# Kernel optimization log

Hardware: AMD Instinct MI355X
Metric: run time of the kernel (lower is better)

The kernel has to match this reference:

```python
import jax, jax.numpy as jnp
import numpy as np

HEADS = 12
DIM_HEAD = 64
WINDOW = 16
SHIFT = 1  # fixed stand-in for random.randint(0, window-1)
SCALE = DIM_HEAD ** -0.5


def window_cls_mask(n, window, shift):
    # Shifted block-diagonal mask over the n-1 non-CLS tokens, CLS attends/attended everywhere.
    size = n - 1
    idx = jnp.arange(size)
    cur = (idx - shift) % window
    left = jnp.clip(idx - cur, 0, size)
    right = jnp.clip(idx + (window - cur), 0, size)
    i = idx[:, None]  # query position
    wmask = (i >= left[None, :]) & (i < right[None, :])  # [size, size]
    full = jnp.ones((n, n), dtype=bool)
    full = full.at[1:, 1:].set(wmask)
    return full  # [n, n] bool


def setup_inputs() -> dict:
    key = jax.random.key(0)
    k1, k2, k3 = jax.random.split(key, 3)
    b, n, dim = 2, 2049, 768
    inner = HEADS * DIM_HEAD
    return {
        "x": jax.random.normal(k1, (b, n, dim), dtype=jnp.float32),
        "w_qkv": jax.random.normal(k2, (dim, 3 * inner), dtype=jnp.float32) * 0.02,
        "w_out": jax.random.normal(k3, (inner, dim), dtype=jnp.float32) * 0.02,
        "b_out": jnp.zeros((dim,), dtype=jnp.float32),
    }


def reference(x, w_qkv, w_out, b_out):
    b, n, dim = x.shape
    h, d = HEADS, DIM_HEAD
    qkv = x @ w_qkv  # [b, n, 3*h*d]
    q, k, v = jnp.split(qkv, 3, axis=-1)
    # b n (h d) -> b h n d
    reshape = lambda t: t.reshape(b, n, h, d).transpose(0, 2, 1, 3)
    q, k, v = reshape(q), reshape(k), reshape(v)
    dots = jnp.einsum('bhid,bhjd->bhij', q, k) * SCALE  # [b, h, n, n]
    mask = window_cls_mask(n, WINDOW, SHIFT)  # [n, n]
    neg = -jnp.finfo(dots.dtype).max
    dots = jnp.where(mask[None, None], dots, neg)
    attn = jax.nn.softmax(dots, axis=-1)
    out = jnp.einsum('bhij,bhjd->bhid', attn, v)  # [b, h, n, d]
    out = out.transpose(0, 2, 1, 3).reshape(b, n, h * d)
    return out @ w_out + b_out
```

## Files before the change

### kernel.cpp

```cpp
#include <hip/hip_runtime.h>
#include <hip/hip_bf16.h>
#include <math.h>

typedef __attribute__((ext_vector_type(8))) __bf16 bf16x8;
typedef __attribute__((ext_vector_type(4))) float f32x4;

#define HEADS 12
#define DHEAD 64
#define NTOK 2049
#define BATCH 2
#define DIM 768
#define QKV3 2304
#define MROWS 4098
#define MP 4224
#define ATT_SCALE 0.125f
#define BKS 64
#define NSPLIT 33
#define PSTRIDE 68

#define CVT_BLOCKS 1584
#define TQKV_BX 72
#define TQKV_BLOCKS (72 * 24)
#define TOUT_BX 24
#define TOUT_BLOCKS (24 * 24)
#define PREP_BLOCKS (CVT_BLOCKS + TQKV_BLOCKS + TOUT_BLOCKS)
#define WIN_BLOCKS (BATCH * 129 * 3)

__device__ __forceinline__ int xcd_swz(int o, int nwg) {
  const int q = nwg >> 3, r = nwg & 7;
  const int xcd = o & 7, i = o >> 3;
  return (xcd < r ? xcd * (q + 1) : r * (q + 1) + (xcd - r) * q) + i;
}

__global__ __launch_bounds__(256) void prep_kernel(const float* __restrict__ x,
                                                   const float* __restrict__ w_qkv,
                                                   const float* __restrict__ w_out,
                                                   __bf16* __restrict__ xb,
                                                   __bf16* __restrict__ wqkvT,
                                                   __bf16* __restrict__ woutT) {
  __shared__ float tile[32][33];
  const int b = blockIdx.x, tid = threadIdx.x;
  if (b < CVT_BLOCKS) {
    long e = ((long)b * 256 + tid) * 8;
    int row = (int)(e / DIM);
    bf16x8 v;
    if (row < MROWS) {
      const float4 a = *(const float4*)(x + e);
      const float4 c = *(const float4*)(x + e + 4);
      v[0] = (__bf16)a.x; v[1] = (__bf16)a.y; v[2] = (__bf16)a.z; v[3] = (__bf16)a.w;
      v[4] = (__bf16)c.x; v[5] = (__bf16)c.y; v[6] = (__bf16)c.z; v[7] = (__bf16)c.w;
    } else {
#pragma unroll
      for (int j = 0; j < 8; ++j) v[j] = (__bf16)0.f;
    }
    *(bf16x8*)(xb + e) = v;
    return;
  }
  const float* in;
  __bf16* outp;
  int C, bx, by;
  if (b < CVT_BLOCKS + TQKV_BLOCKS) {
    int idx = b - CVT_BLOCKS;
    bx = idx % TQKV_BX; by = idx / TQKV_BX;
    in = w_qkv; outp = wqkvT; C = QKV3;
  } else {
    int idx = b - CVT_BLOCKS - TQKV_BLOCKS;
    bx = idx % TOUT_BX; by = idx / TOUT_BX;
    in = w_out; outp = woutT; C = DIM;
  }
  const int R = DIM;
  const int c0 = bx * 32, r0 = by * 32;
  const int tx = tid & 31, ty = tid >> 5;
#pragma unroll
  for (int i = 0; i < 4; ++i) {
    int r = ty + i * 8;
    tile[r][tx] = in[(size_t)(r0 + r) * C + c0 + tx];
  }
  __syncthreads();
#pragma unroll
  for (int i = 0; i < 4; ++i) {
    int r = ty + i * 8;
    outp[(size_t)(c0 + r) * R + r0 + tx] = (__bf16)tile[tx][r];
  }
}

__global__ __launch_bounds__(256) void gemm_qkv_kernel(const __bf16* __restrict__ A,
                                                       const __bf16* __restrict__ Bt,
                                                       __bf16* __restrict__ C) {
  __shared__ __bf16 sA[2][64 * BKS];
  __shared__ __bf16 sB[2][128 * BKS];
  const int wg = xcd_swz(blockIdx.x, (MP / 64) * (QKV3 / 128));
  const int by = wg / (QKV3 / 128), bx = wg % (QKV3 / 128);
  const int tid = threadIdx.x;
  const int w = tid >> 6, lane = tid & 63;
  const int m0 = by * 64, n0 = bx * 128;
  const int wr = w >> 1, wc = w & 1;
  const int K = DIM;
  f32x4 acc[2][4] = {};

  const int srow = (w << 3) + (lane >> 3);
  const int scolE = ((lane & 7) ^ (lane >> 3)) << 3;
  const __bf16* gA = A + (size_t)(m0 + srow) * K + scolE;
  const __bf16* gB = Bt + (size_t)(n0 + srow) * K + scolE;
  const int nk = K / BKS;

#define STAGE_Q(buf, kt)                                                                 \
  do {                                                                                   \
    _Pragma("unroll")                                                                    \
    for (int it = 0; it < 2; ++it) {                                                     \
      __builtin_amdgcn_global_load_lds(                                                  \
          (const __attribute__((address_space(1))) void*)(gA + (size_t)(it * 32) * K + (kt)), \
          (__attribute__((address_space(3))) void*)(&sA[buf][(it << 11) + (w << 9)]), 16, 0, 0); \
    }                                                                                    \
    _Pragma("unroll")                                                                    \
    for (int it = 0; it < 4; ++it) {                                                     \
      __builtin_amdgcn_global_load_lds(                                                  \
          (const __attribute__((address_space(1))) void*)(gB + (size_t)(it * 32) * K + (kt)), \
          (__attribute__((address_space(3))) void*)(&sB[buf][(it << 11) + (w << 9)]), 16, 0, 0); \
    }                                                                                    \
  } while (0)

  STAGE_Q(0, 0);
  __syncthreads();

  const int sw0 = ((lane >> 4) ^ (lane & 7)) << 3;
  const int sw1 = sw0 ^ 32;
  const int rofA = (wr * 32 + (lane & 15)) * BKS;
  const int rofB = (wc * 64 + (lane & 15)) * BKS;

  for (int t = 0; t < nk; ++t) {
    const int cur = t & 1;
    if (t + 1 < nk) STAGE_Q(cur ^ 1, (t + 1) * BKS);
    const __bf16* bufA = sA[cur];
    const __bf16* bufB = sB[cur];
#pragma unroll
    for (int kk = 0; kk < BKS; kk += 32) {
      const int so = (kk == 0) ? sw0 : sw1;
      bf16x8 af[2], bfr[4];
#pragma unroll
      for (int m = 0; m < 2; ++m)
        af[m] = *(const bf16x8*)&bufA[rofA + m * 16 * BKS + so];
#pragma unroll
      for (int n = 0; n < 4; ++n)
        bfr[n] = *(const bf16x8*)&bufB[rofB + n * 16 * BKS + so];
#pragma unroll
      for (int m = 0; m < 2; ++m)
#pragma unroll
        for (int n = 0; n < 4; ++n)
          acc[m][n] = __builtin_amdgcn_mfma_f32_16x16x32_bf16(af[m], bfr[n], acc[m][n], 0, 0, 0);
    }
    __syncthreads();
  }
#undef STAGE_Q

#pragma unroll
  for (int m = 0; m < 2; ++m) {
#pragma unroll
    for (int n = 0; n < 4; ++n) {
      int col = n0 + wc * 64 + n * 16 + (lane & 15);
      int rbase = m0 + wr * 32 + m * 16 + ((lane >> 4) << 2);
#pragma unroll
      for (int r = 0; r < 4; ++r) {
        C[(size_t)(rbase + r) * QKV3 + col] = (__bf16)acc[m][n][r];
      }
    }
  }
}

__global__ __launch_bounds__(256) void gemm_out_kernel(const __bf16* __restrict__ A,
                                                       const __bf16* __restrict__ Bt,
                                                       float* __restrict__ Cv,
                                                       const float* __restrict__ bias) {
  __shared__ __bf16 sA[2][64 * BKS];
  __shared__ __bf16 sB[2][64 * BKS];
  const int wg = xcd_swz(blockIdx.x, (MP / 64) * (DIM / 64));
  const int by = wg / (DIM / 64), bx = wg % (DIM / 64);
  const int tid = threadIdx.x;
  const int w = tid >> 6, lane = tid & 63;
  const int m0 = by * 64, n0 = bx * 64;
  const int wr = w >> 1, wc = w & 1;
  const int K = DIM, N = DIM;
  f32x4 acc[2][2] = {};

  const int srow = (w << 3) + (lane >> 3);
  const int scol = ((lane & 7) ^ (lane >> 3)) << 3;
  const __bf16* gA = A + (size_t)(m0 + srow) * K + scol;
  const __bf16* gB = Bt + (size_t)(n0 + srow) * K + scol;
  const int nk = K / BKS;

#define STAGE_O(buf, kt)                                                                 \
  do {                                                                                   \
    _Pragma("unroll")                                                                    \
    for (int it = 0; it < 2; ++it) {                                                     \
      __builtin_amdgcn_global_load_lds(                                                  \
          (const __attribute__((address_space(1))) void*)(gA + (size_t)(it * 32) * K + (kt)), \
          (__attribute__((address_space(3))) void*)(&sA[buf][(it << 11) + (w << 9)]), 16, 0, 0); \
      __builtin_amdgcn_global_load_lds(                                                  \
          (const __attribute__((address_space(1))) void*)(gB + (size_t)(it * 32) * K + (kt)), \
          (__attribute__((address_space(3))) void*)(&sB[buf][(it << 11) + (w << 9)]), 16, 0, 0); \
    }                                                                                    \
  } while (0)

  STAGE_O(0, 0);
  __syncthreads();

  const int sw0 = ((lane >> 4) ^ (lane & 7)) << 3;
  const int sw1 = sw0 ^ 32;
  const int rofA = (wr * 32 + (lane & 15)) * BKS;
  const int rofB = (wc * 32 + (lane & 15)) * BKS;

  for (int t = 0; t < nk; ++t) {
    const int cur = t & 1;
    if (t + 1 < nk) STAGE_O(cur ^ 1, (t + 1) * BKS);
    const __bf16* bufA = sA[cur];
    const __bf16* bufB = sB[cur];
#pragma unroll
    for (int kk = 0; kk < BKS; kk += 32) {
      const int so = (kk == 0) ? sw0 : sw1;
      bf16x8 af[2], bfr[2];
#pragma unroll
      for (int m = 0; m < 2; ++m)
        af[m] = *(const bf16x8*)&bufA[rofA + m * 16 * BKS + so];
#pragma unroll
      for (int n = 0; n < 2; ++n)
        bfr[n] = *(const bf16x8*)&bufB[rofB + n * 16 * BKS + so];
#pragma unroll
      for (int m = 0; m < 2; ++m)
#pragma unroll
        for (int n = 0; n < 2; ++n)
          acc[m][n] = __builtin_amdgcn_mfma_f32_16x16x32_bf16(af[m], bfr[n], acc[m][n], 0, 0, 0);
    }
    __syncthreads();
  }
#undef STAGE_O

#pragma unroll
  for (int m = 0; m < 2; ++m) {
#pragma unroll
    for (int n = 0; n < 2; ++n) {
      int col = n0 + wc * 32 + n * 16 + (lane & 15);
      int rbase = m0 + wr * 32 + m * 16 + ((lane >> 4) << 2);
#pragma unroll
      for (int r = 0; r < 4; ++r) {
        int row = rbase + r;
        if (row < MROWS) Cv[(size_t)row * N + col] = acc[m][n][r] + bias[col];
      }
    }
  }
}

__global__ __launch_bounds__(64) void attn_fused_kernel(const __bf16* __restrict__ qkv,
                                                        __bf16* __restrict__ attnb,
                                                        float* __restrict__ part) {
  __shared__ float sp_lds[64];
  const int lane = threadIdx.x;

  if (blockIdx.x < WIN_BLOCKS) {
    int bidx = blockIdx.x;
    int hg = bidx % 3; bidx /= 3;
    int blk = bidx % 129;
    int bb = bidx / 129;
    int h = hg * 4 + (lane >> 4);
    int qi = lane & 15;
    int t0 = (blk == 0) ? 1 : 2 + 16 * (blk - 1);
    int nt = (blk == 0) ? 1 : ((NTOK - t0) < 16 ? (NTOK - t0) : 16);
    bool active = qi < nt;
    int qt = t0 + (active ? qi : nt - 1);
    const size_t base = (size_t)bb * NTOK * QKV3;

    float q[64];
    {
      const __bf16* qp = qkv + base + (size_t)qt * QKV3 + h * DHEAD;
#pragma unroll
      for (int d0 = 0; d0 < 64; d0 += 8) {
        bf16x8 v = *(const bf16x8*)(qp + d0);
#pragma unroll
        for (int j = 0; j < 8; ++j) q[d0 + j] = (float)v[j];
      }
    }

    float s[17];
    float mx = -3.4e38f;
#pragma unroll
    for (int j = 0; j < 17; ++j) {
      int jc = (j - 1) < (nt - 1) ? (j - 1) : (nt - 1);
      int kt = (j == 0) ? 0 : t0 + jc;
      const __bf16* kp = qkv + base + (size_t)kt * QKV3 + DIM + h * DHEAD;
      float dot = 0.f;
#pragma unroll
      for (int d0 = 0; d0 < 64; d0 += 8) {
        bf16x8 v = *(const bf16x8*)(kp + d0);
#pragma unroll
        for (int jj = 0; jj < 8; ++jj) dot = fmaf(q[d0 + jj], (float)v[jj], dot);
      }
      s[j] = (j <= nt) ? dot * ATT_SCALE : -3.4e38f;
      mx = fmaxf(mx, s[j]);
    }
    float sum = 0.f;
#pragma unroll
    for (int j = 0; j < 17; ++j) {
      s[j] = expf(s[j] - mx);
      sum += s[j];
    }
    float inv = 1.f / sum;

    float o[64];
#pragma unroll
    for (int d = 0; d < 64; ++d) o[d] = 0.f;
#pragma unroll
    for (int j = 0; j < 17; ++j) {
      int jc = (j - 1) < (nt - 1) ? (j - 1) : (nt - 1);
      int vt = (j == 0) ? 0 : t0 + jc;
      const __bf16* vp = qkv + base + (size_t)vt * QKV3 + 2 * DIM + h * DHEAD;
      float p = s[j];
#pragma unroll
      for (int d0 = 0; d0 < 64; d0 += 8) {
        bf16x8 v = *(const bf16x8*)(vp + d0);
#pragma unroll
        for (int jj = 0; jj < 8; ++jj) o[d0 + jj] = fmaf(p, (float)v[jj], o[d0 + jj]);
      }
    }

    if (active) {
      __bf16* op = attnb + (size_t)(bb * NTOK + qt) * DIM + h * DHEAD;
#pragma unroll
      for (int d0 = 0; d0 < 64; d0 += 8) {
        bf16x8 v;
#pragma unroll
        for (int j = 0; j < 8; ++j) v[j] = (__bf16)(o[d0 + j] * inv);
        *(bf16x8*)(op + d0) = v;
      }
    }
    return;
  }

  int bid = blockIdx.x - WIN_BLOCKS;
  const int sp = bid % NSPLIT;
  const int bh = bid / NSPLIT;
  const int h = bh % HEADS;
  const int bb = bh / HEADS;
  const size_t base = (size_t)bb * NTOK * QKV3;

  float q[64];
  {
    const __bf16* qp = qkv + base + h * DHEAD;
#pragma unroll
    for (int d0 = 0; d0 < 64; d0 += 8) {
      bf16x8 v = *(const bf16x8*)(qp + d0);
#pragma unroll
      for (int j = 0; j < 8; ++j) q[d0 + j] = (float)v[j];
    }
  }

  const int t = sp * 64 + lane;
  const bool valid = t < NTOK;
  const int tc = valid ? t : NTOK - 1;
  float dot = 0.f;
  {
    const __bf16* kp = qkv + base + (size_t)tc * QKV3 + DIM + h * DHEAD;
#pragma unroll
    for (int d0 = 0; d0 < 64; d0 += 8) {
      bf16x8 v = *(const bf16x8*)(kp + d0);
#pragma unroll
      for (int j = 0; j < 8; ++j) dot = fmaf(q[d0 + j], (float)v[j], dot);
    }
  }
  float s = valid ? dot * ATT_SCALE : -3.4e38f;

  float m = s;
#pragma unroll
  for (int off = 32; off > 0; off >>= 1) m = fmaxf(m, __shfl_xor(m, off, 64));
  float p = valid ? expf(s - m) : 0.f;
  float l = p;
#pragma unroll
  for (int off = 32; off > 0; off >>= 1) l += __shfl_xor(l, off, 64);

  sp_lds[lane] = p;
  __syncthreads();

  const int nt = (NTOK - sp * 64) < 64 ? (NTOK - sp * 64) : 64;
  float o = 0.f;
  const __bf16* vcol = qkv + base + (size_t)(sp * 64) * QKV3 + 2 * DIM + h * DHEAD + lane;
  for (int tt = 0; tt < nt; ++tt) {
    o = fmaf(sp_lds[tt], (float)vcol[(size_t)tt * QKV3], o);
  }

  float* pb = part + ((size_t)bh * NSPLIT + sp) * PSTRIDE;
  pb[lane] = o;
  if (lane == 0) { pb[64] = m; pb[65] = l; }
}

__global__ __launch_bounds__(64) void attn_cls_reduce(const float* __restrict__ part,
                                                      __bf16* __restrict__ attnb) {
  const int bh = blockIdx.x;
  const int h = bh % HEADS;
  const int bb = bh / HEADS;
  const int lane = threadIdx.x;
  const float* pb0 = part + (size_t)bh * NSPLIT * PSTRIDE;
  float M = -3.4e38f;
#pragma unroll
  for (int i = 0; i < NSPLIT; ++i) M = fmaxf(M, pb0[i * PSTRIDE + 64]);
  float L = 0.f, o = 0.f;
#pragma unroll
  for (int i = 0; i < NSPLIT; ++i) {
    float w = expf(pb0[i * PSTRIDE + 64] - M);
    L = fmaf(pb0[i * PSTRIDE + 65], w, L);
    o = fmaf(pb0[i * PSTRIDE + lane], w, o);
  }
  attnb[(size_t)(bb * NTOK) * DIM + h * DHEAD + lane] = (__bf16)(o / L);
}

extern "C" void kernel_launch(void* const* d_in, const int* in_sizes, int n_in,
                              void* d_out, int out_size, void* d_ws, size_t ws_size,
                              hipStream_t stream) {
  const float* x = (const float*)d_in[0];
  const float* w_qkv = (const float*)d_in[1];
  const float* w_out = (const float*)d_in[2];
  const float* b_out = (const float*)d_in[3];
  float* out = (float*)d_out;

  char* ws = (char*)d_ws;
  __bf16* xb    = (__bf16*)(ws);
  __bf16* wqkvT = (__bf16*)(ws + 6488064);
  __bf16* woutT = (__bf16*)(ws + 6488064 + 3538944);
  __bf16* qkvb  = (__bf16*)(ws + 6488064 + 3538944 + 1179648);
  __bf16* attnb = (__bf16*)(ws + 6488064 + 3538944 + 1179648 + 19464192);
  float*  clsp  = (float*)(ws + 6488064 + 3538944 + 1179648 + 19464192 + 6488064);

  prep_kernel<<<PREP_BLOCKS, 256, 0, stream>>>(x, w_qkv, w_out, xb, wqkvT, woutT);

  gemm_qkv_kernel<<<(MP / 64) * (QKV3 / 128), 256, 0, stream>>>(xb, wqkvT, qkvb);

  attn_fused_kernel<<<WIN_BLOCKS + BATCH * HEADS * NSPLIT, 64, 0, stream>>>(qkvb, attnb, clsp);
  attn_cls_reduce<<<BATCH * HEADS, 64, 0, stream>>>(clsp, attnb);

  gemm_out_kernel<<<(MP / 64) * (DIM / 64), 256, 0, stream>>>(attnb, woutT, out, b_out);
}
```

Measured before the change: 149.0 us.

## Stage window K/V in LDS and fold CLS reduction into attention via atomic counter

```diff
diff --git a/kernel.cpp b/kernel.cpp
--- a/kernel.cpp
+++ b/kernel.cpp
@@ -37,9 +37,11 @@
                                                    const float* __restrict__ w_out,
                                                    __bf16* __restrict__ xb,
                                                    __bf16* __restrict__ wqkvT,
-                                                   __bf16* __restrict__ woutT) {
+                                                   __bf16* __restrict__ woutT,
+                                                   int* __restrict__ cnt) {
   __shared__ float tile[32][33];
   const int b = blockIdx.x, tid = threadIdx.x;
+  if (b == 0 && tid < BATCH * HEADS) cnt[tid] = 0;
   if (b < CVT_BLOCKS) {
     long e = ((long)b * 256 + tid) * 8;
     int row = (int)(e / DIM);
@@ -251,7 +253,10 @@
 
 __global__ __launch_bounds__(64) void attn_fused_kernel(const __bf16* __restrict__ qkv,
                                                         __bf16* __restrict__ attnb,
-                                                        float* __restrict__ part) {
+                                                        float* __restrict__ part,
+                                                        int* __restrict__ cnt) {
+  __shared__ __bf16 sK[17 * 256];
+  __shared__ __bf16 sV[17 * 256];
   __shared__ float sp_lds[64];
   const int lane = threadIdx.x;
 
@@ -268,6 +273,17 @@
     int qt = t0 + (active ? qi : nt - 1);
     const size_t base = (size_t)bb * NTOK * QKV3;
 
+    const int hlw = lane >> 4;
+    const int colw = hlw * 64 + (((lane & 15) * 4 + hlw * 16) & 63);
+#pragma unroll
+    for (int r = 0; r < 17; ++r) {
+      int tok = (r == 0) ? 0 : t0 + ((r - 1) < (nt - 1) ? (r - 1) : (nt - 1));
+      const ushort* kp = (const ushort*)(qkv + base + (size_t)tok * QKV3 + DIM) + hg * 256;
+      *(ushort4*)&sK[r * 256 + colw] = *(const ushort4*)(kp + (lane << 2));
+      *(ushort4*)&sV[r * 256 + colw] = *(const ushort4*)(kp + DIM + (lane << 2));
+    }
+    __syncthreads();
+
     float q[64];
     {
       const __bf16* qp = qkv + base + (size_t)qt * QKV3 + h * DHEAD;
@@ -279,17 +295,16 @@
       }
     }
 
+    const int hl = lane >> 4;
     float s[17];
     float mx = -3.4e38f;
 #pragma unroll
     for (int j = 0; j < 17; ++j) {
-      int jc = (j - 1) < (nt - 1) ? (j - 1) : (nt - 1);
-      int kt = (j == 0) ? 0 : t0 + jc;
-      const __bf16* kp = qkv + base + (size_t)kt * QKV3 + DIM + h * DHEAD;
       float dot = 0.f;
 #pragma unroll
       for (int d0 = 0; d0 < 64; d0 += 8) {
-        bf16x8 v = *(const bf16x8*)(kp + d0);
+        const int col = hl * 64 + ((d0 + hl * 16) & 63);
+        bf16x8 v = *(const bf16x8*)&sK[j * 256 + col];
 #pragma unroll
         for (int jj = 0; jj < 8; ++jj) dot = fmaf(q[d0 + jj], (float)v[jj], dot);
       }
@@ -309,13 +324,11 @@
     for (int d = 0; d < 64; ++d) o[d] = 0.f;
 #pragma unroll
     for (int j = 0; j < 17; ++j) {
-      int jc = (j - 1) < (nt - 1) ? (j - 1) : (nt - 1);
-      int vt = (j == 0) ? 0 : t0 + jc;
-      const __bf16* vp = qkv + base + (size_t)vt * QKV3 + 2 * DIM + h * DHEAD;
       float p = s[j];
 #pragma unroll
       for (int d0 = 0; d0 < 64; d0 += 8) {
-        bf16x8 v = *(const bf16x8*)(vp + d0);
+        const int col = hl * 64 + ((d0 + hl * 16) & 63);
+        bf16x8 v = *(const bf16x8*)&sV[j * 256 + col];
 #pragma unroll
         for (int jj = 0; jj < 8; ++jj) o[d0 + jj] = fmaf(p, (float)v[jj], o[d0 + jj]);
       }
@@ -388,26 +401,26 @@
   float* pb = part + ((size_t)bh * NSPLIT + sp) * PSTRIDE;
   pb[lane] = o;
   if (lane == 0) { pb[64] = m; pb[65] = l; }
-}
-
-__global__ __launch_bounds__(64) void attn_cls_reduce(const float* __restrict__ part,
-                                                      __bf16* __restrict__ attnb) {
-  const int bh = blockIdx.x;
-  const int h = bh % HEADS;
-  const int bb = bh / HEADS;
-  const int lane = threadIdx.x;
+
+  __threadfence();
+  int last = 0;
+  if (lane == 0) last = (atomicAdd(&cnt[bh], 1) == NSPLIT - 1) ? 1 : 0;
+  last = __shfl(last, 0, 64);
+  if (!last) return;
+  __threadfence();
+
   const float* pb0 = part + (size_t)bh * NSPLIT * PSTRIDE;
   float M = -3.4e38f;
 #pragma unroll
   for (int i = 0; i < NSPLIT; ++i) M = fmaxf(M, pb0[i * PSTRIDE + 64]);
-  float L = 0.f, o = 0.f;
+  float L = 0.f, oo = 0.f;
 #pragma unroll
   for (int i = 0; i < NSPLIT; ++i) {
     float w = expf(pb0[i * PSTRIDE + 64] - M);
     L = fmaf(pb0[i * PSTRIDE + 65], w, L);
-    o = fmaf(pb0[i * PSTRIDE + lane], w, o);
-  }
-  attnb[(size_t)(bb * NTOK) * DIM + h * DHEAD + lane] = (__bf16)(o / L);
+    oo = fmaf(pb0[i * PSTRIDE + lane], w, oo);
+  }
+  attnb[(size_t)(bb * NTOK) * DIM + h * DHEAD + lane] = (__bf16)(oo / L);
 }
 
 extern "C" void kernel_launch(void* const* d_in, const int* in_sizes, int n_in,
@@ -425,14 +438,14 @@
   __bf16* woutT = (__bf16*)(ws + 6488064 + 3538944);
   __bf16* qkvb  = (__bf16*)(ws + 6488064 + 3538944 + 1179648);
   __bf16* attnb = (__bf16*)(ws + 6488064 + 3538944 + 1179648 + 19464192);
-  float*  clsp  = (float*)(ws + 6488064 + 3538944 + 1179648 + 19464192 + 6488064);
-
-  prep_kernel<<<PREP_BLOCKS, 256, 0, stream>>>(x, w_qkv, w_out, xb, wqkvT, woutT);
+  int*    cnt   = (int*)  (ws + 6488064 + 3538944 + 1179648 + 19464192 + 6488064);
+  float*  clsp  = (float*)(ws + 6488064 + 3538944 + 1179648 + 19464192 + 6488064 + 512);
+
+  prep_kernel<<<PREP_BLOCKS, 256, 0, stream>>>(x, w_qkv, w_out, xb, wqkvT, woutT, cnt);
 
   gemm_qkv_kernel<<<(MP / 64) * (QKV3 / 128), 256, 0, stream>>>(xb, wqkvT, qkvb);
 
-  attn_fused_kernel<<<WIN_BLOCKS + BATCH * HEADS * NSPLIT, 64, 0, stream>>>(qkvb, attnb, clsp);
-  attn_cls_reduce<<<BATCH * HEADS, 64, 0, stream>>>(clsp, attnb);
+  attn_fused_kernel<<<WIN_BLOCKS + BATCH * HEADS * NSPLIT, 64, 0, stream>>>(qkvb, attnb, clsp, cnt);
 
   gemm_out_kernel<<<(MP / 64) * (DIM / 64), 256, 0, stream>>>(attnb, woutT, out, b_out);
 }
```

After: 177.5 us. +19.1%, slower.

## Split head dimension across four lanes in windowed attention path

Applied to the files above, without the earlier changes.

```diff
diff --git a/kernel.cpp b/kernel.cpp
--- a/kernel.cpp
+++ b/kernel.cpp
@@ -24,7 +24,7 @@
 #define TOUT_BX 24
 #define TOUT_BLOCKS (24 * 24)
 #define PREP_BLOCKS (CVT_BLOCKS + TQKV_BLOCKS + TOUT_BLOCKS)
-#define WIN_BLOCKS (BATCH * 129 * 3)
+#define WIN_BLOCKS (BATCH * 129 * HEADS)
 
 __device__ __forceinline__ int xcd_swz(int o, int nwg) {
   const int q = nwg >> 3, r = nwg & 7;
@@ -257,26 +257,25 @@
 
   if (blockIdx.x < WIN_BLOCKS) {
     int bidx = blockIdx.x;
-    int hg = bidx % 3; bidx /= 3;
-    int blk = bidx % 129;
-    int bb = bidx / 129;
-    int h = hg * 4 + (lane >> 4);
-    int qi = lane & 15;
-    int t0 = (blk == 0) ? 1 : 2 + 16 * (blk - 1);
-    int nt = (blk == 0) ? 1 : ((NTOK - t0) < 16 ? (NTOK - t0) : 16);
-    bool active = qi < nt;
-    int qt = t0 + (active ? qi : nt - 1);
+    const int h = bidx % HEADS; bidx /= HEADS;
+    const int blk = bidx % 129;
+    const int bb = bidx / 129;
+    const int qi = lane >> 2;
+    const int dq = lane & 3;
+    const int t0 = (blk == 0) ? 1 : 2 + 16 * (blk - 1);
+    const int nt = (blk == 0) ? 1 : ((NTOK - t0) < 16 ? (NTOK - t0) : 16);
+    const bool active = qi < nt;
+    const int qt = t0 + (active ? qi : nt - 1);
     const size_t base = (size_t)bb * NTOK * QKV3;
-
-    float q[64];
+    const int dbase = h * DHEAD + dq * 16;
+
+    float q[16];
     {
-      const __bf16* qp = qkv + base + (size_t)qt * QKV3 + h * DHEAD;
-#pragma unroll
-      for (int d0 = 0; d0 < 64; d0 += 8) {
-        bf16x8 v = *(const bf16x8*)(qp + d0);
-#pragma unroll
-        for (int j = 0; j < 8; ++j) q[d0 + j] = (float)v[j];
-      }
+      const __bf16* qp = qkv + base + (size_t)qt * QKV3 + dbase;
+      bf16x8 v0 = *(const bf16x8*)qp;
+      bf16x8 v1 = *(const bf16x8*)(qp + 8);
+#pragma unroll
+      for (int j = 0; j < 8; ++j) { q[j] = (float)v0[j]; q[8 + j] = (float)v1[j]; }
     }
 
     float s[17];
@@ -285,14 +284,17 @@
     for (int j = 0; j < 17; ++j) {
       int jc = (j - 1) < (nt - 1) ? (j - 1) : (nt - 1);
       int kt = (j == 0) ? 0 : t0 + jc;
-      const __bf16* kp = qkv + base + (size_t)kt * QKV3 + DIM + h * DHEAD;
+      const __bf16* kp = qkv + base + (size_t)kt * QKV3 + DIM + dbase;
+      bf16x8 v0 = *(const bf16x8*)kp;
+      bf16x8 v1 = *(const bf16x8*)(kp + 8);
       float dot = 0.f;
 #pragma unroll
-      for (int d0 = 0; d0 < 64; d0 += 8) {
-        bf16x8 v = *(const bf16x8*)(kp + d0);
-#pragma unroll
-        for (int jj = 0; jj < 8; ++jj) dot = fmaf(q[d0 + jj], (float)v[jj], dot);
+      for (int jj = 0; jj < 8; ++jj) {
+        dot = fmaf(q[jj], (float)v0[jj], dot);
+        dot = fmaf(q[8 + jj], (float)v1[jj], dot);
       }
+      dot += __shfl_xor(dot, 1, 64);
+      dot += __shfl_xor(dot, 2, 64);
       s[j] = (j <= nt) ? dot * ATT_SCALE : -3.4e38f;
       mx = fmaxf(mx, s[j]);
     }
@@ -304,32 +306,34 @@
     }
     float inv = 1.f / sum;
 
-    float o[64];
-#pragma unroll
-    for (int d = 0; d < 64; ++d) o[d] = 0.f;
+    float o[16];
+#pragma unroll
+    for (int d = 0; d < 16; ++d) o[d] = 0.f;
 #pragma unroll
     for (int j = 0; j < 17; ++j) {
       int jc = (j - 1) < (nt - 1) ? (j - 1) : (nt - 1);
       int vt = (j == 0) ? 0 : t0 + jc;
-      const __bf16* vp = qkv + base + (size_t)vt * QKV3 + 2 * DIM + h * DHEAD;
+      const __bf16* vp = qkv + base + (size_t)vt * QKV3 + 2 * DIM + dbase;
+      bf16x8 v0 = *(const bf16x8*)vp;
+      bf16x8 v1 = *(const bf16x8*)(vp + 8);
       float p = s[j];
 #pragma unroll
-      for (int d0 = 0; d0 < 64; d0 += 8) {
-        bf16x8 v = *(const bf16x8*)(vp + d0);
-#pragma unroll
-        for (int jj = 0; jj < 8; ++jj) o[d0 + jj] = fmaf(p, (float)v[jj], o[d0 + jj]);
+      for (int jj = 0; jj < 8; ++jj) {
+        o[jj] = fmaf(p, (float)v0[jj], o[jj]);
+        o[8 + jj] = fmaf(p, (float)v1[jj], o[8 + jj]);
       }
     }
 
     if (active) {
-      __bf16* op = attnb + (size_t)(bb * NTOK + qt) * DIM + h * DHEAD;
-#pragma unroll
-      for (int d0 = 0; d0 < 64; d0 += 8) {
-        bf16x8 v;
-#pragma unroll
-        for (int j = 0; j < 8; ++j) v[j] = (__bf16)(o[d0 + j] * inv);
-        *(bf16x8*)(op + d0) = v;
+      __bf16* op = attnb + (size_t)(bb * NTOK + qt) * DIM + dbase;
+      bf16x8 w0, w1;
+#pragma unroll
+      for (int j = 0; j < 8; ++j) {
+        w0[j] = (__bf16)(o[j] * inv);
+        w1[j] = (__bf16)(o[8 + j] * inv);
       }
+      *(bf16x8*)op = w0;
+      *(bf16x8*)(op + 8) = w1;
     }
     return;
   }
```

After: 140.9 us. -5.5%, faster.
